# Kernel optimization log

Measured on AMD Instinct MI355X. Metric: run time of the kernel, lower is better.

Reference implementation:

```python
import jax, jax.numpy as jnp
import numpy as np

B, T_NEW, CACHED_MAX = 8, 128, 2048
D_MODEL, N_HEADS = 1024, 16
D_HEAD = D_MODEL // N_HEADS
MAX_TOTAL = CACHED_MAX + T_NEW


def rotate_half(x):
    x1, x2 = x[..., : x.shape[-1] // 2], x[..., x.shape[-1] // 2 :]
    return jnp.concatenate([-x2, x1], axis=-1)


def setup_inputs() -> dict:
    key = jax.random.key(0)
    ks = jax.random.split(key, 16)
    w_scale = D_MODEL ** -0.5  # xavier-ish
    inp = {
        "x_new": jax.random.normal(ks[0], (B, T_NEW, D_MODEL), jnp.float32),
        "past_k": jax.random.normal(ks[1], (B, N_HEADS, CACHED_MAX, D_HEAD), jnp.float32),
        "past_v": jax.random.normal(ks[2], (B, N_HEADS, CACHED_MAX, D_HEAD), jnp.float32),
        "Wq": jax.random.normal(ks[3], (D_MODEL, D_MODEL), jnp.float32) * w_scale,
        "bq": jnp.zeros((D_MODEL,), jnp.float32),
        "Wk": jax.random.normal(ks[4], (D_MODEL, D_MODEL), jnp.float32) * w_scale,
        "bk": jnp.zeros((D_MODEL,), jnp.float32),
        "Wv": jax.random.normal(ks[5], (D_MODEL, D_MODEL), jnp.float32) * w_scale,
        "bv": jnp.zeros((D_MODEL,), jnp.float32),
        "Wo": jax.random.normal(ks[6], (D_MODEL, D_MODEL), jnp.float32) * w_scale,
        "bo": jnp.zeros((D_MODEL,), jnp.float32),
        "inv_freq": 1.0 / (10000.0 ** (jnp.arange(0, D_HEAD, 2, dtype=jnp.float32) / D_HEAD)),
        # ragged lengths; >=1 so every row attends to something
        "past_lengths": jax.random.randint(ks[7], (B,), 1, CACHED_MAX + 1),
        "new_lengths": jax.random.randint(ks[8], (B,), 1, T_NEW + 1),
    }
    return inp


def _attention_fwd(x_new, past_k, past_v, Wq, bq, Wk, bk, Wv, bv, Wo, bo, inv_freq,
                   past_lengths, new_lengths):
    steps = jnp.arange(T_NEW)
    valid_new = steps[None, :] < new_lengths[:, None]            # [B, T_new]

    def proj(W, b):  # torch Linear: x @ W.T + b -> [B, H, T_new, D_head]
        y = jnp.einsum("btm,nm->btn", x_new, W) + b
        return y.reshape(B, T_NEW, N_HEADS, D_HEAD).transpose(0, 2, 1, 3)

    q, k_new, v_new = proj(Wq, bq), proj(Wk, bk), proj(Wv, bv)

    # RoPE at absolute positions past_len + step (0 where invalid)
    positions = jnp.where(valid_new, past_lengths[:, None] + steps[None, :], 0)
    freqs = positions[..., None].astype(jnp.float32) * inv_freq  # [B, T_new, D_head/2]
    emb = jnp.concatenate([freqs, freqs], axis=-1)               # [B, T_new, D_head]
    cos = jnp.cos(emb)[:, None]                                  # [B, 1, T_new, D_head]
    sin = jnp.sin(emb)[:, None]
    q = q * cos + rotate_half(q) * sin
    k_new = k_new * cos + rotate_half(k_new) * sin

    vm = valid_new[:, None, :, None].astype(q.dtype)
    q, k_new, v_new = q * vm, k_new * vm, v_new * vm

    total_lengths = past_lengths + new_lengths
    j = jnp.arange(MAX_TOTAL)
    in_past = (j[None, :] < past_lengths[:, None])[:, None, :, None]       # [B,1,MT,1]
    in_new = ((j[None, :] >= past_lengths[:, None]) &
              (j[None, :] < total_lengths[:, None]))[:, None, :, None]
    idx_new = jnp.clip(j[None, :] - past_lengths[:, None], 0, T_NEW - 1)   # [B, MT]

    past_k_pad = jnp.pad(past_k, ((0, 0), (0, 0), (0, T_NEW), (0, 0)))
    past_v_pad = jnp.pad(past_v, ((0, 0), (0, 0), (0, T_NEW), (0, 0)))
    gather = jax.vmap(lambda xb, ib: xb[:, ib])  # [H,T_new,D], [MT] -> [H,MT,D]
    k_total = jnp.where(in_past, past_k_pad, jnp.where(in_new, gather(k_new, idx_new), 0.0))
    v_total = jnp.where(in_past, past_v_pad, jnp.where(in_new, gather(v_new, idx_new), 0.0))

    attend = j[None, :] < total_lengths[:, None]                  # [B, MT]
    scores = jnp.einsum("bhqd,bhkd->bhqk", q, k_total) * (D_HEAD ** -0.5)
    neg = jnp.asarray(jnp.finfo(scores.dtype).min, scores.dtype)
    scores = jnp.where(attend[:, None, None, :], scores, neg)
    attn = jax.nn.softmax(scores, axis=-1)
    ctx = jnp.einsum("bhqk,bhkd->bhqd", attn, v_total)            # [B,H,T_new,D]

    out = ctx.transpose(0, 2, 1, 3).reshape(B, T_NEW, D_MODEL)
    out = jnp.einsum("btm,nm->btn", out, Wo) + bo
    return out * valid_new[..., None].astype(out.dtype)


def reference(x_new, past_k, past_v, Wq, bq, Wk, bk, Wv, bv, Wo, bo, inv_freq,
              past_lengths, new_lengths):
    return _attention_fwd(x_new, past_k, past_v, Wq, bq, Wk, bk, Wv, bv, Wo, bo,
                          inv_freq, past_lengths, new_lengths)
```

## Files before the change

kernel.cpp:

```cpp
#include <hip/hip_runtime.h>

#define NB 8
#define TNEW 128
#define CMAX 2048
#define DMODEL 1024
#define NH 16
#define DH 64

typedef float f32x4 __attribute__((ext_vector_type(4)));
typedef short short8 __attribute__((ext_vector_type(8)));
typedef short short4v __attribute__((ext_vector_type(4)));
typedef unsigned uint4v __attribute__((ext_vector_type(4)));

__device__ __forceinline__ short f2bf(float x) {
  unsigned u = __float_as_uint(x);
  u += 0x7FFFu + ((u >> 16) & 1u);
  return (short)(u >> 16);
}
__device__ __forceinline__ float bf2f(short s) {
  return __uint_as_float(((unsigned)(unsigned short)s) << 16);
}
__device__ __forceinline__ short8 cvt8(f32x4 a, f32x4 b) {
  uint4v t;
  asm("v_cvt_pk_bf16_f32 %0, %1, %2" : "=v"(t.x) : "v"(a.x), "v"(a.y));
  asm("v_cvt_pk_bf16_f32 %0, %1, %2" : "=v"(t.y) : "v"(a.z), "v"(a.w));
  asm("v_cvt_pk_bf16_f32 %0, %1, %2" : "=v"(t.z) : "v"(b.x), "v"(b.y));
  asm("v_cvt_pk_bf16_f32 %0, %1, %2" : "=v"(t.w) : "v"(b.z), "v"(b.w));
  return __builtin_bit_cast(short8, t);
}

#define LGKM0_BAR()                                            \
  __builtin_amdgcn_sched_barrier(0);                           \
  asm volatile("s_waitcnt lgkmcnt(0)" ::: "memory");           \
  __builtin_amdgcn_sched_barrier(0);                           \
  __builtin_amdgcn_s_barrier()
#define TAIL_BAR()                                             \
  __builtin_amdgcn_sched_barrier(0);                           \
  __builtin_amdgcn_s_barrier()

__global__ __launch_bounds__(256) void cvt5_bf16(
    const float* __restrict__ s0, const float* __restrict__ s1,
    const float* __restrict__ s2, const float* __restrict__ s3,
    const float* __restrict__ s4, short* __restrict__ dst) {
  const int seg = blockIdx.x >> 10;
  const int i = (blockIdx.x & 1023) * 256 + threadIdx.x;
  const float* src = seg == 0 ? s0 : seg == 1 ? s1 : seg == 2 ? s2 : seg == 3 ? s3 : s4;
  f32x4 v = *(const f32x4*)(src + (size_t)i * 4);
  short4v o;
  o.x = f2bf(v.x); o.y = f2bf(v.y); o.z = f2bf(v.z); o.w = f2bf(v.w);
  *(short4v*)(dst + (size_t)seg * (1u << 20) + (size_t)i * 4) = o;
}

__global__ __launch_bounds__(256) void gemm64(
    const short* __restrict__ A, const short* __restrict__ Wbase,
    void* __restrict__ Out, const float* __restrict__ bias0,
    const float* __restrict__ bias1, const float* __restrict__ bias2,
    const int* __restrict__ new_len, const float* __restrict__ inv_freq,
    const int* __restrict__ past_len)
{
  constexpr int LDT = 40;
  __shared__ short As[64 * LDT];
  __shared__ short Bs[64 * LDT];
  const int n0 = blockIdx.x * 64, m0 = blockIdx.y * 64, z = blockIdx.z;
  if ((m0 & 64) && new_len[m0 >> 7] <= 64) return;
  const short* Wp = Wbase + (size_t)z * (DMODEL * DMODEL);
  const float* bias = z == 0 ? bias0 : (z == 1 ? bias1 : bias2);
  const int tid = threadIdx.x, lane = tid & 63, w = tid >> 6;
  const int wm = (w >> 1) * 32, wn2 = (w & 1) * 16;
  const int lr = lane & 15, lk = lane >> 4;

  const int srow = tid >> 2, soff = (tid & 3) * 8;
  const short* Ag = A  + (size_t)(m0 + srow) * DMODEL + soff;
  const short* Bg = Wp + (size_t)(n0 + srow) * DMODEL + soff;
  short* Al = As + srow * LDT + soff;
  short* Bl = Bs + srow * LDT + soff;

  short8 va0 = *(const short8*)(Ag);
  short8 vb0 = *(const short8*)(Bg);
  short8 va1, vb1;
  f32x4 acc[2][2] = {};

#define GEMM_PHASE(CURA, CURB, NXTA, NXTB, KNEXT)                          \
  {                                                                        \
    *(short8*)Al = CURA;                                                   \
    *(short8*)Bl = CURB;                                                   \
    NXTA = *(const short8*)(Ag + (KNEXT) * 32);                            \
    NXTB = *(const short8*)(Bg + (KNEXT) * 32);                            \
    LGKM0_BAR();                                                           \
    short8 af0 = *(const short8*)(As + (wm + lr) * LDT + lk * 8);          \
    short8 af1 = *(const short8*)(As + (wm + 16 + lr) * LDT + lk * 8);     \
    short8 bg0 = *(const short8*)(Bs + (wn2 + lr) * LDT + lk * 8);         \
    short8 bg1 = *(const short8*)(Bs + (wn2 + 32 + lr) * LDT + lk * 8);    \
    acc[0][0] = __builtin_amdgcn_mfma_f32_16x16x32_bf16(af0, bg0, acc[0][0], 0, 0, 0); \
    acc[0][1] = __builtin_amdgcn_mfma_f32_16x16x32_bf16(af0, bg1, acc[0][1], 0, 0, 0); \
    acc[1][0] = __builtin_amdgcn_mfma_f32_16x16x32_bf16(af1, bg0, acc[1][0], 0, 0, 0); \
    acc[1][1] = __builtin_amdgcn_mfma_f32_16x16x32_bf16(af1, bg1, acc[1][1], 0, 0, 0); \
    TAIL_BAR();                                                            \
  }

  for (int kt = 0; kt < DMODEL / 32; kt += 2) {
    const int k1 = kt + 1;
    const int k2 = (kt + 2 < DMODEL / 32) ? kt + 2 : DMODEL / 32 - 1;
    GEMM_PHASE(va0, vb0, va1, vb1, k1);
    GEMM_PHASE(va1, vb1, va0, vb0, k2);
  }
#undef GEMM_PHASE

  const int colb = n0 + wn2 + lr;
  const float b0 = bias[colb], b1 = bias[colb + 32];
  short* outp = (short*)Out + (size_t)z * (NB * TNEW * DMODEL);

  if (z <= 1) {
    const int pbase = past_len[m0 >> 7];
    const float fr = inv_freq[(wn2 + lr) & 31];
#pragma unroll
    for (int i = 0; i < 2; ++i) {
#pragma unroll
      for (int r = 0; r < 4; ++r) {
        const int row = m0 + wm + i * 16 + lk * 4 + r;
        const float pos = (float)(pbase + (row & 127));
        float sn, cs;
        __sincosf(pos * fr, &sn, &cs);
        const float a0 = acc[i][0][r] + b0;
        const float a1 = acc[i][1][r] + b1;
        outp[(size_t)row * DMODEL + colb]      = f2bf(a0 * cs - a1 * sn);
        outp[(size_t)row * DMODEL + colb + 32] = f2bf(a1 * cs + a0 * sn);
      }
    }
  } else {
#pragma unroll
    for (int i = 0; i < 2; ++i) {
#pragma unroll
      for (int r = 0; r < 4; ++r) {
        const int row = m0 + wm + i * 16 + lk * 4 + r;
        outp[(size_t)row * DMODEL + colb]      = f2bf(acc[i][0][r] + b0);
        outp[(size_t)row * DMODEL + colb + 32] = f2bf(acc[i][1][r] + b1);
      }
    }
  }
}

__global__ __launch_bounds__(256) void outproj64(
    const short* __restrict__ A, const short* __restrict__ W,
    float* __restrict__ Out, const float* __restrict__ bias,
    const int* __restrict__ new_len)
{
  constexpr int LDT = 40;
  __shared__ short As[64 * LDT];
  __shared__ short Bs[64 * LDT];
  const int n0 = blockIdx.x * 64, m0 = blockIdx.y * 64;
  const int nlen = new_len[m0 >> 7];
  if ((m0 & 64) && nlen <= 64) {
    const int rr = threadIdx.x >> 2, cc = (threadIdx.x & 3) * 16;
    const f32x4 z4 = {};
#pragma unroll
    for (int u = 0; u < 4; ++u)
      *(f32x4*)(&Out[(size_t)(m0 + rr) * DMODEL + n0 + cc + u * 4]) = z4;
    return;
  }
  const int tid = threadIdx.x, lane = tid & 63, w = tid >> 6;
  const int wm = (w >> 1) * 32, wn2 = (w & 1) * 16;
  const int lr = lane & 15, lk = lane >> 4;

  const int srow = tid >> 2, soff = (tid & 3) * 8;
  const short* Ag = A + (size_t)(m0 + srow) * DMODEL + soff;
  const short* Bg = W + (size_t)(n0 + srow) * DMODEL + soff;
  short* Al = As + srow * LDT + soff;
  short* Bl = Bs + srow * LDT + soff;

  short8 va0 = *(const short8*)(Ag);
  short8 vb0 = *(const short8*)(Bg);
  short8 va1, vb1;
  f32x4 acc[2][2] = {};

#define GEMM_PHASE(CURA, CURB, NXTA, NXTB, KNEXT)                          \
  {                                                                        \
    *(short8*)Al = CURA;                                                   \
    *(short8*)Bl = CURB;                                                   \
    NXTA = *(const short8*)(Ag + (KNEXT) * 32);                            \
    NXTB = *(const short8*)(Bg + (KNEXT) * 32);                            \
    LGKM0_BAR();                                                           \
    short8 af0 = *(const short8*)(As + (wm + lr) * LDT + lk * 8);          \
    short8 af1 = *(const short8*)(As + (wm + 16 + lr) * LDT + lk * 8);     \
    short8 bg0 = *(const short8*)(Bs + (wn2 + lr) * LDT + lk * 8);         \
    short8 bg1 = *(const short8*)(Bs + (wn2 + 32 + lr) * LDT + lk * 8);    \
    acc[0][0] = __builtin_amdgcn_mfma_f32_16x16x32_bf16(af0, bg0, acc[0][0], 0, 0, 0); \
    acc[0][1] = __builtin_amdgcn_mfma_f32_16x16x32_bf16(af0, bg1, acc[0][1], 0, 0, 0); \
    acc[1][0] = __builtin_amdgcn_mfma_f32_16x16x32_bf16(af1, bg0, acc[1][0], 0, 0, 0); \
    acc[1][1] = __builtin_amdgcn_mfma_f32_16x16x32_bf16(af1, bg1, acc[1][1], 0, 0, 0); \
    TAIL_BAR();                                                            \
  }

  for (int kt = 0; kt < DMODEL / 32; kt += 2) {
    const int k1 = kt + 1;
    const int k2 = (kt + 2 < DMODEL / 32) ? kt + 2 : DMODEL / 32 - 1;
    GEMM_PHASE(va0, vb0, va1, vb1, k1);
    GEMM_PHASE(va1, vb1, va0, vb0, k2);
  }
#undef GEMM_PHASE

  const int colb = n0 + wn2 + lr;
  const float b0 = bias[colb], b1 = bias[colb + 32];
#pragma unroll
  for (int i = 0; i < 2; ++i)
#pragma unroll
    for (int r = 0; r < 4; ++r) {
      const int row = m0 + wm + i * 16 + lk * 4 + r;
      const bool ok = (row & 127) < nlen;
      Out[(size_t)row * DMODEL + colb]      = ok ? acc[i][0][r] + b0 : 0.0f;
      Out[(size_t)row * DMODEL + colb + 32] = ok ? acc[i][1][r] + b1 : 0.0f;
    }
}

__global__ __launch_bounds__(512, 4) void attn_split(
    const float* __restrict__ pk, const float* __restrict__ pv,
    const short* __restrict__ qb, const short* __restrict__ kb,
    const short* __restrict__ vb, float* __restrict__ Opart,
    float* __restrict__ Ml, const int* __restrict__ past_len,
    const int* __restrict__ new_len, int splits)
{
  constexpr int LDT = 72;
  __shared__ short Kl[64 * LDT];
  __shared__ short Vt[64 * LDT];
  __shared__ short Pl[128 * LDT];
  const int id = blockIdx.x;
  const int bh = id / splits, s = id - bh * splits;
  const int b = bh >> 4, h = bh & 15;
  const int past = past_len[b];
  const int nlen = new_len[b];
  const int total = past + nlen;
  const int tid = threadIdx.x, lane = tid & 63, w = tid >> 6;
  const int lr = lane & 15, lk = lane >> 4;

  const int nt = (total + 63) >> 6;

  float* mlp = Ml + (size_t)(bh * splits + s) * 256;
  float* op  = Opart + (size_t)(bh * splits + s) * (128 * 64);

  if (s >= nt) {
#pragma unroll
    for (int r = 0; r < 4; ++r) {
      const int q = w * 16 + lk * 4 + r;
      if (lr == 0) { mlp[q] = -3.0e38f; mlp[128 + q] = 0.f; }
    }
    return;
  }

  const bool wvalid = (w * 16) < nlen;
  short8 qf0 = {}, qf1 = {};
  if (wvalid) {
    const short* qrow = qb + (size_t)(b * 128 + w * 16 + lr) * DMODEL + h * 64;
    qf0 = *(const short8*)(qrow + lk * 8);
    qf1 = *(const short8*)(qrow + 32 + lk * 8);
  }
  float m_run[4], l_run[4];
  f32x4 acc[4] = {};
#pragma unroll
  for (int r = 0; r < 4; ++r) { m_run[r] = -3.0e38f; l_run[r] = 0.f; }

  const int jr = tid >> 3, seg = tid & 7;
  const float* pkb = pk + ((size_t)(b * 16 + h) * CMAX) * 64 + seg * 8;
  const float* pvb = pv + ((size_t)(b * 16 + h) * CMAX) * 64 + seg * 8;
  const short* kbb = kb + (size_t)(b * 128) * DMODEL + h * 64 + seg * 8;
  const short* vbb = vb + (size_t)(b * 128) * DMODEL + h * 64 + seg * 8;

  f32x4 kF0, kF1, vF0, vF1;
  short8 kN, vN;
  int tmode;
  bool pr0, pr1;

#define STAGE_ISSUE(T)                                                        \
  {                                                                           \
    const int t0_ = (T) * 64;                                                 \
    if (t0_ + 64 <= past) {                                                   \
      tmode = 0;                                                              \
      const int j_ = t0_ + jr;                                                \
      kF0 = *(const f32x4*)(pkb + (size_t)j_ * 64);                           \
      kF1 = *(const f32x4*)(pkb + (size_t)j_ * 64 + 4);                       \
      vF0 = *(const f32x4*)(pvb + (size_t)j_ * 64);                           \
      vF1 = *(const f32x4*)(pvb + (size_t)j_ * 64 + 4);                       \
    } else if (t0_ >= past && t0_ + 64 <= total) {                            \
      tmode = 1;                                                              \
      const int jn = t0_ + jr - past;                                         \
      kN = *(const short8*)(kbb + (size_t)jn * DMODEL);                       \
      vN = *(const short8*)(vbb + (size_t)jn * DMODEL);                       \
    } else {                                                                  \
      tmode = 2;                                                              \
      const int j_ = t0_ + jr;                                                \
      const int jp = min(j_, past - 1);                 \
      const int jn = min(max(j_ - past, 0), TNEW - 1);                        \
      pr0 = j_ < past;                                                        \
      pr1 = j_ < total;                                                       \
      kF0 = *(const f32x4*)(pkb + (size_t)jp * 64);                           \
      kF1 = *(const f32x4*)(pkb + (size_t)jp * 64 + 4);                       \
      vF0 = *(const f32x4*)(pvb + (size_t)jp * 64);                           \
      vF1 = *(const f32x4*)(pvb + (size_t)jp * 64 + 4);                       \
      kN  = *(const short8*)(kbb + (size_t)jn * DMODEL);                      \
      vN  = *(const short8*)(vbb + (size_t)jn * DMODEL);                      \
    }                                                                         \
  }

  STAGE_ISSUE(s);
  for (int kt = s; kt < nt; kt += splits) {
    {
      const int pmode = tmode;
      const bool qr0 = pr0, qr1 = pr1;
      short8 kr, vr;
      if (pmode == 0) {
        kr = cvt8(kF0, kF1);
        vr = cvt8(vF0, vF1);
      } else if (pmode == 1) {
        kr = kN;
        vr = vN;
      } else {
        const short8 z8 = {};
        short8 kc = cvt8(kF0, kF1);
        short8 vc = cvt8(vF0, vF1);
        kr = qr0 ? kc : (qr1 ? kN : z8);
        vr = qr0 ? vc : (qr1 ? vN : z8);
      }
      *(short8*)(Kl + jr * LDT + seg * 8) = kr;
#pragma unroll
      for (int i = 0; i < 8; ++i) Vt[(seg * 8 + i) * LDT + (jr ^ (seg * 8))] = vr[i];
    }
    STAGE_ISSUE(kt + splits);
    LGKM0_BAR();

    if (wvalid) {
      f32x4 sc[4];
      __builtin_amdgcn_s_setprio(1);
#pragma unroll
      for (int nf = 0; nf < 4; ++nf) {
        short8 k0 = *(const short8*)(Kl + (nf * 16 + lr) * LDT + lk * 8);
        short8 k1 = *(const short8*)(Kl + (nf * 16 + lr) * LDT + 32 + lk * 8);
        f32x4 zv = {};
        zv = __builtin_amdgcn_mfma_f32_16x16x32_bf16(qf0, k0, zv, 0, 0, 0);
        sc[nf] = __builtin_amdgcn_mfma_f32_16x16x32_bf16(qf1, k1, zv, 0, 0, 0);
      }
      __builtin_amdgcn_s_setprio(0);
      const int kg0 = kt * 64;
      float pmax[4] = {-3.0e38f, -3.0e38f, -3.0e38f, -3.0e38f};
#pragma unroll
      for (int nf = 0; nf < 4; ++nf) {
        const bool ok = (kg0 + nf * 16 + lr) < total;
#pragma unroll
        for (int r = 0; r < 4; ++r) {
          const float sv = ok ? sc[nf][r] * 0.125f : -3.0e38f;
          sc[nf][r] = sv;
          pmax[r] = fmaxf(pmax[r], sv);
        }
      }
#pragma unroll
      for (int r = 0; r < 4; ++r) {
#pragma unroll
        for (int off = 1; off < 16; off <<= 1)
          pmax[r] = fmaxf(pmax[r], __shfl_xor(pmax[r], off));
      }
      float alpha[4], rsum[4];
#pragma unroll
      for (int r = 0; r < 4; ++r) {
        const float mn = fmaxf(m_run[r], pmax[r]);
        alpha[r] = __expf(m_run[r] - mn);
        m_run[r] = mn;
        rsum[r] = 0.f;
      }
#pragma unroll
      for (int nf = 0; nf < 4; ++nf)
#pragma unroll
        for (int r = 0; r < 4; ++r) {
          const float p = __expf(sc[nf][r] - m_run[r]);
          sc[nf][r] = p;
          rsum[r] += p;
        }
#pragma unroll
      for (int r = 0; r < 4; ++r) {
#pragma unroll
        for (int off = 1; off < 16; off <<= 1)
          rsum[r] += __shfl_xor(rsum[r], off);
        l_run[r] = l_run[r] * alpha[r] + rsum[r];
      }
#pragma unroll
      for (int nf = 0; nf < 4; ++nf)
#pragma unroll
        for (int r = 0; r < 4; ++r) acc[nf][r] *= alpha[r];

#pragma unroll
      for (int nf = 0; nf < 4; ++nf)
#pragma unroll
        for (int r = 0; r < 4; ++r)
          Pl[(w * 16 + lk * 4 + r) * LDT + nf * 16 + lr] = f2bf(sc[nf][r]);
      __builtin_amdgcn_s_setprio(1);
#pragma unroll
      for (int kf = 0; kf < 2; ++kf) {
        short8 pf = *(const short8*)(Pl + (w * 16 + lr) * LDT + kf * 32 + lk * 8);
#pragma unroll
        for (int nf = 0; nf < 4; ++nf) {
          const int dd = nf * 16 + lr;
          short8 vf = *(const short8*)(Vt + dd * LDT + ((kf * 32 + lk * 8) ^ (dd & 56)));
          acc[nf] = __builtin_amdgcn_mfma_f32_16x16x32_bf16(pf, vf, acc[nf], 0, 0, 0);
        }
      }
      __builtin_amdgcn_s_setprio(0);
    }
    TAIL_BAR();
  }
#undef STAGE_ISSUE

  if (wvalid) {
#pragma unroll
    for (int nf = 0; nf < 4; ++nf)
#pragma unroll
      for (int r = 0; r < 4; ++r) {
        const int q = w * 16 + lk * 4 + r, d = nf * 16 + lr;
        op[(size_t)q * 64 + d] = acc[nf][r];
      }
#pragma unroll
    for (int r = 0; r < 4; ++r) {
      const int q = w * 16 + lk * 4 + r;
      if (lr == 0) { mlp[q] = m_run[r]; mlp[128 + q] = l_run[r]; }
    }
  } else {
#pragma unroll
    for (int r = 0; r < 4; ++r) {
      const int q = w * 16 + lk * 4 + r;
      if (lr == 0) { mlp[q] = -3.0e38f; mlp[128 + q] = 0.f; }
    }
  }
}

__global__ __launch_bounds__(256) void attn_combine(
    const float* __restrict__ Opart, const float* __restrict__ Ml,
    short* __restrict__ ctxb, const int* __restrict__ new_len, int splits)
{
  const int bh = blockIdx.x, b = bh >> 4, h = bh & 15;
  const int q = blockIdx.y * 16 + (threadIdx.x >> 4);
  if (q >= new_len[b]) return;
  const int dv = (threadIdx.x & 15) * 4;
  const float* mlb = Ml + (size_t)bh * splits * 256;
  float mstar = -3.0e38f;
  for (int s = 0; s < splits; ++s)
    mstar = fmaxf(mstar, mlb[s * 256 + q]);
  float lsum = 0.f;
  f32x4 o = {};
  for (int s = 0; s < splits; ++s) {
    const float ws = __expf(mlb[s * 256 + q] - mstar);
    lsum += ws * mlb[s * 256 + 128 + q];
    if (ws > 0.f) {
      f32x4 ov = *(const f32x4*)(Opart + ((size_t)(bh * splits + s) * 128 + q) * 64 + dv);
      o.x += ws * ov.x; o.y += ws * ov.y; o.z += ws * ov.z; o.w += ws * ov.w;
    }
  }
  const float inv = 1.0f / lsum;
  short4v r;
  r.x = f2bf(o.x * inv); r.y = f2bf(o.y * inv); r.z = f2bf(o.z * inv); r.w = f2bf(o.w * inv);
  *(short4v*)(ctxb + (size_t)(b * 128 + q) * DMODEL + h * 64 + dv) = r;
}

extern "C" void kernel_launch(void* const* d_in, const int* in_sizes, int n_in,
                              void* d_out, int out_size, void* d_ws, size_t ws_size,
                              hipStream_t stream) {
  const float* x      = (const float*)d_in[0];
  const float* past_k = (const float*)d_in[1];
  const float* past_v = (const float*)d_in[2];
  const float* Wq = (const float*)d_in[3];
  const float* bq = (const float*)d_in[4];
  const float* Wk = (const float*)d_in[5];
  const float* bk = (const float*)d_in[6];
  const float* Wv = (const float*)d_in[7];
  const float* bv = (const float*)d_in[8];
  const float* Wo = (const float*)d_in[9];
  const float* bo = (const float*)d_in[10];
  const float* inv_freq = (const float*)d_in[11];
  const int* past_len = (const int*)d_in[12];
  const int* new_len  = (const int*)d_in[13];

  short* wsb = (short*)d_ws;
  const size_t M1 = 1u << 20;
  short* Xb  = wsb;
  short* Wqb = wsb + 1 * M1;
  short* Wob = wsb + 4 * M1;
  short* qb  = wsb + 5 * M1;
  short* kb  = wsb + 6 * M1;
  short* vb  = wsb + 7 * M1;
  short* ctx = wsb + 8 * M1;
  float* Opart = (float*)(wsb + 9 * M1);

  int splits = 1;
  for (int s = 8; s >= 1; s >>= 1) {
    size_t need = 9 * M1 * sizeof(short) +
                  (size_t)s * 128 * (128 * 64 + 256) * sizeof(float);
    if (need <= ws_size) { splits = s; break; }
  }
  float* Ml = Opart + (size_t)128 * splits * (128 * 64);

  cvt5_bf16<<<5120, 256, 0, stream>>>(x, Wq, Wk, Wv, Wo, wsb);

  gemm64<<<dim3(16, 16, 3), 256, 0, stream>>>(Xb, Wqb, (void*)qb, bq, bk, bv,
                                              new_len, inv_freq, past_len);
  attn_split<<<128 * splits, 512, 0, stream>>>(past_k, past_v, qb, kb, vb,
                                               Opart, Ml, past_len, new_len, splits);
  attn_combine<<<dim3(128, 8), 256, 0, stream>>>(Opart, Ml, ctx, new_len, splits);
  outproj64<<<dim3(16, 16), 256, 0, stream>>>(ctx, Wob, (float*)d_out, bo, new_len);
}
```

Before: 69.01 us.

## Deepen GEMM k-step, add lazy softmax rescaling, allow more attention splits

```diff
diff --git a/kernel.cpp b/kernel.cpp
--- a/kernel.cpp
+++ b/kernel.cpp
@@ -59,8 +59,8 @@
     const int* __restrict__ past_len)
 {
   constexpr int LDT = 40;
-  __shared__ short As[64 * LDT];
-  __shared__ short Bs[64 * LDT];
+  __shared__ short As[2][64 * LDT];
+  __shared__ short Bs[2][64 * LDT];
   const int n0 = blockIdx.x * 64, m0 = blockIdx.y * 64, z = blockIdx.z;
   if ((m0 & 64) && new_len[m0 >> 7] <= 64) return;
   const short* Wp = Wbase + (size_t)z * (DMODEL * DMODEL);
@@ -72,39 +72,41 @@
   const int srow = tid >> 2, soff = (tid & 3) * 8;
   const short* Ag = A  + (size_t)(m0 + srow) * DMODEL + soff;
   const short* Bg = Wp + (size_t)(n0 + srow) * DMODEL + soff;
-  short* Al = As + srow * LDT + soff;
-  short* Bl = Bs + srow * LDT + soff;
+  short* Al0 = &As[0][srow * LDT + soff];
+  short* Bl0 = &Bs[0][srow * LDT + soff];
+  short* Al1 = &As[1][srow * LDT + soff];
+  short* Bl1 = &Bs[1][srow * LDT + soff];
 
   short8 va0 = *(const short8*)(Ag);
   short8 vb0 = *(const short8*)(Bg);
-  short8 va1, vb1;
+  short8 va1 = *(const short8*)(Ag + 32);
+  short8 vb1 = *(const short8*)(Bg + 32);
   f32x4 acc[2][2] = {};
 
-#define GEMM_PHASE(CURA, CURB, NXTA, NXTB, KNEXT)                          \
-  {                                                                        \
-    *(short8*)Al = CURA;                                                   \
-    *(short8*)Bl = CURB;                                                   \
-    NXTA = *(const short8*)(Ag + (KNEXT) * 32);                            \
-    NXTB = *(const short8*)(Bg + (KNEXT) * 32);                            \
-    LGKM0_BAR();                                                           \
-    short8 af0 = *(const short8*)(As + (wm + lr) * LDT + lk * 8);          \
-    short8 af1 = *(const short8*)(As + (wm + 16 + lr) * LDT + lk * 8);     \
-    short8 bg0 = *(const short8*)(Bs + (wn2 + lr) * LDT + lk * 8);         \
-    short8 bg1 = *(const short8*)(Bs + (wn2 + 32 + lr) * LDT + lk * 8);    \
-    acc[0][0] = __builtin_amdgcn_mfma_f32_16x16x32_bf16(af0, bg0, acc[0][0], 0, 0, 0); \
-    acc[0][1] = __builtin_amdgcn_mfma_f32_16x16x32_bf16(af0, bg1, acc[0][1], 0, 0, 0); \
-    acc[1][0] = __builtin_amdgcn_mfma_f32_16x16x32_bf16(af1, bg0, acc[1][0], 0, 0, 0); \
-    acc[1][1] = __builtin_amdgcn_mfma_f32_16x16x32_bf16(af1, bg1, acc[1][1], 0, 0, 0); \
-    TAIL_BAR();                                                            \
-  }
-
-  for (int kt = 0; kt < DMODEL / 32; kt += 2) {
-    const int k1 = kt + 1;
-    const int k2 = (kt + 2 < DMODEL / 32) ? kt + 2 : DMODEL / 32 - 1;
-    GEMM_PHASE(va0, vb0, va1, vb1, k1);
-    GEMM_PHASE(va1, vb1, va0, vb0, k2);
-  }
-#undef GEMM_PHASE
+  for (int it = 0; it < 16; ++it) {
+    *(short8*)Al0 = va0;
+    *(short8*)Bl0 = vb0;
+    *(short8*)Al1 = va1;
+    *(short8*)Bl1 = vb1;
+    const int kn = (it < 15 ? 2 * it + 2 : 30) * 32;
+    va0 = *(const short8*)(Ag + kn);
+    vb0 = *(const short8*)(Bg + kn);
+    va1 = *(const short8*)(Ag + kn + 32);
+    vb1 = *(const short8*)(Bg + kn + 32);
+    LGKM0_BAR();
+#pragma unroll
+    for (int sb = 0; sb < 2; ++sb) {
+      short8 af0 = *(const short8*)(&As[sb][(wm + lr) * LDT + lk * 8]);
+      short8 af1 = *(const short8*)(&As[sb][(wm + 16 + lr) * LDT + lk * 8]);
+      short8 bg0 = *(const short8*)(&Bs[sb][(wn2 + lr) * LDT + lk * 8]);
+      short8 bg1 = *(const short8*)(&Bs[sb][(wn2 + 32 + lr) * LDT + lk * 8]);
+      acc[0][0] = __builtin_amdgcn_mfma_f32_16x16x32_bf16(af0, bg0, acc[0][0], 0, 0, 0);
+      acc[0][1] = __builtin_amdgcn_mfma_f32_16x16x32_bf16(af0, bg1, acc[0][1], 0, 0, 0);
+      acc[1][0] = __builtin_amdgcn_mfma_f32_16x16x32_bf16(af1, bg0, acc[1][0], 0, 0, 0);
+      acc[1][1] = __builtin_amdgcn_mfma_f32_16x16x32_bf16(af1, bg1, acc[1][1], 0, 0, 0);
+    }
+    TAIL_BAR();
+  }
 
   const int colb = n0 + wn2 + lr;
   const float b0 = bias[colb], b1 = bias[colb + 32];
@@ -146,8 +148,8 @@
     const int* __restrict__ new_len)
 {
   constexpr int LDT = 40;
-  __shared__ short As[64 * LDT];
-  __shared__ short Bs[64 * LDT];
+  __shared__ short As[2][64 * LDT];
+  __shared__ short Bs[2][64 * LDT];
   const int n0 = blockIdx.x * 64, m0 = blockIdx.y * 64;
   const int nlen = new_len[m0 >> 7];
   if ((m0 & 64) && nlen <= 64) {
@@ -165,39 +167,41 @@
   const int srow = tid >> 2, soff = (tid & 3) * 8;
   const short* Ag = A + (size_t)(m0 + srow) * DMODEL + soff;
   const short* Bg = W + (size_t)(n0 + srow) * DMODEL + soff;
-  short* Al = As + srow * LDT + soff;
-  short* Bl = Bs + srow * LDT + soff;
+  short* Al0 = &As[0][srow * LDT + soff];
+  short* Bl0 = &Bs[0][srow * LDT + soff];
+  short* Al1 = &As[1][srow * LDT + soff];
+  short* Bl1 = &Bs[1][srow * LDT + soff];
 
   short8 va0 = *(const short8*)(Ag);
   short8 vb0 = *(const short8*)(Bg);
-  short8 va1, vb1;
+  short8 va1 = *(const short8*)(Ag + 32);
+  short8 vb1 = *(const short8*)(Bg + 32);
   f32x4 acc[2][2] = {};
 
-#define GEMM_PHASE(CURA, CURB, NXTA, NXTB, KNEXT)                          \
-  {                                                                        \
-    *(short8*)Al = CURA;                                                   \
-    *(short8*)Bl = CURB;                                                   \
-    NXTA = *(const short8*)(Ag + (KNEXT) * 32);                            \
-    NXTB = *(const short8*)(Bg + (KNEXT) * 32);                            \
-    LGKM0_BAR();                                                           \
-    short8 af0 = *(const short8*)(As + (wm + lr) * LDT + lk * 8);          \
-    short8 af1 = *(const short8*)(As + (wm + 16 + lr) * LDT + lk * 8);     \
-    short8 bg0 = *(const short8*)(Bs + (wn2 + lr) * LDT + lk * 8);         \
-    short8 bg1 = *(const short8*)(Bs + (wn2 + 32 + lr) * LDT + lk * 8);    \
-    acc[0][0] = __builtin_amdgcn_mfma_f32_16x16x32_bf16(af0, bg0, acc[0][0], 0, 0, 0); \
-    acc[0][1] = __builtin_amdgcn_mfma_f32_16x16x32_bf16(af0, bg1, acc[0][1], 0, 0, 0); \
-    acc[1][0] = __builtin_amdgcn_mfma_f32_16x16x32_bf16(af1, bg0, acc[1][0], 0, 0, 0); \
-    acc[1][1] = __builtin_amdgcn_mfma_f32_16x16x32_bf16(af1, bg1, acc[1][1], 0, 0, 0); \
-    TAIL_BAR();                                                            \
-  }
-
-  for (int kt = 0; kt < DMODEL / 32; kt += 2) {
-    const int k1 = kt + 1;
-    const int k2 = (kt + 2 < DMODEL / 32) ? kt + 2 : DMODEL / 32 - 1;
-    GEMM_PHASE(va0, vb0, va1, vb1, k1);
-    GEMM_PHASE(va1, vb1, va0, vb0, k2);
-  }
-#undef GEMM_PHASE
+  for (int it = 0; it < 16; ++it) {
+    *(short8*)Al0 = va0;
+    *(short8*)Bl0 = vb0;
+    *(short8*)Al1 = va1;
+    *(short8*)Bl1 = vb1;
+    const int kn = (it < 15 ? 2 * it + 2 : 30) * 32;
+    va0 = *(const short8*)(Ag + kn);
+    vb0 = *(const short8*)(Bg + kn);
+    va1 = *(const short8*)(Ag + kn + 32);
+    vb1 = *(const short8*)(Bg + kn + 32);
+    LGKM0_BAR();
+#pragma unroll
+    for (int sb = 0; sb < 2; ++sb) {
+      short8 af0 = *(const short8*)(&As[sb][(wm + lr) * LDT + lk * 8]);
+      short8 af1 = *(const short8*)(&As[sb][(wm + 16 + lr) * LDT + lk * 8]);
+      short8 bg0 = *(const short8*)(&Bs[sb][(wn2 + lr) * LDT + lk * 8]);
+      short8 bg1 = *(const short8*)(&Bs[sb][(wn2 + 32 + lr) * LDT + lk * 8]);
+      acc[0][0] = __builtin_amdgcn_mfma_f32_16x16x32_bf16(af0, bg0, acc[0][0], 0, 0, 0);
+      acc[0][1] = __builtin_amdgcn_mfma_f32_16x16x32_bf16(af0, bg1, acc[0][1], 0, 0, 0);
+      acc[1][0] = __builtin_amdgcn_mfma_f32_16x16x32_bf16(af1, bg0, acc[1][0], 0, 0, 0);
+      acc[1][1] = __builtin_amdgcn_mfma_f32_16x16x32_bf16(af1, bg1, acc[1][1], 0, 0, 0);
+    }
+    TAIL_BAR();
+  }
 
   const int colb = n0 + wn2 + lr;
   const float b0 = bias[colb], b1 = bias[colb + 32];
@@ -356,14 +360,24 @@
         for (int off = 1; off < 16; off <<= 1)
           pmax[r] = fmaxf(pmax[r], __shfl_xor(pmax[r], off));
       }
-      float alpha[4], rsum[4];
+      float mx[4];
+      bool need = false;
 #pragma unroll
       for (int r = 0; r < 4; ++r) {
-        const float mn = fmaxf(m_run[r], pmax[r]);
-        alpha[r] = __expf(m_run[r] - mn);
-        m_run[r] = mn;
-        rsum[r] = 0.f;
-      }
+        mx[r] = fmaxf(m_run[r], pmax[r]);
+        need = need || (pmax[r] > m_run[r] + 8.0f);
+      }
+      if (__any(need)) {
+#pragma unroll
+        for (int r = 0; r < 4; ++r) {
+          const float al = __expf(m_run[r] - mx[r]);
+          m_run[r] = mx[r];
+          l_run[r] *= al;
+#pragma unroll
+          for (int nf = 0; nf < 4; ++nf) acc[nf][r] *= al;
+        }
+      }
+      float rsum[4] = {0.f, 0.f, 0.f, 0.f};
 #pragma unroll
       for (int nf = 0; nf < 4; ++nf)
 #pragma unroll
@@ -377,12 +391,8 @@
 #pragma unroll
         for (int off = 1; off < 16; off <<= 1)
           rsum[r] += __shfl_xor(rsum[r], off);
-        l_run[r] = l_run[r] * alpha[r] + rsum[r];
-      }
-#pragma unroll
-      for (int nf = 0; nf < 4; ++nf)
-#pragma unroll
-        for (int r = 0; r < 4; ++r) acc[nf][r] *= alpha[r];
+        l_run[r] += rsum[r];
+      }
 
 #pragma unroll
       for (int nf = 0; nf < 4; ++nf)
@@ -486,7 +496,7 @@
   float* Opart = (float*)(wsb + 9 * M1);
 
   int splits = 1;
-  for (int s = 8; s >= 1; s >>= 1) {
+  for (int s = 16; s >= 1; s >>= 1) {
     size_t need = 9 * M1 * sizeof(short) +
                   (size_t)s * 128 * (128 * 64 + 256) * sizeof(float);
     if (need <= ws_size) { splits = s; break; }
```

Result: slower. 75.05 us (+8.8%).
